# Kernel optimization log

Measured on AMD Instinct MI355X. Metric: run time of the kernel, lower is better.

The kernel has to match this reference:

```python
import jax, jax.numpy as jnp
import numpy as np

# Tap patterns inside the 3x3 window (ky, kx) for each kernel_type.
# kernel_type=0 'skel' (5 taps): cross (center + 4-neighborhood).
SKEL_TAPS = [(0, 1), (1, 0), (1, 1), (1, 2), (2, 1)]


def build_dense_kernel(weight, taps):
    # weight: [O, C, K] sparse-tap weights -> dense [K*O, C, 3, 3] conv kernel,
    # kernel-major channel layout (j*O + o) to match torch.cat over tap dim.
    O, C, K = weight.shape
    dense = jnp.zeros((K, O, C, 3, 3), dtype=weight.dtype)
    for j, (ky, kx) in enumerate(taps):  # K is small and fixed (5)
        dense = dense.at[j, :, :, ky, kx].set(weight[:, :, j])
    return dense.reshape(K * O, C, 3, 3)


def setup_inputs() -> dict:
    key = jax.random.key(0)
    k1, k2 = jax.random.split(key)
    x = jax.random.normal(k1, (32, 128, 64, 64), dtype=jnp.float32)
    weight = jax.random.normal(k2, (128, 128, 5), dtype=jnp.float32) * 0.05
    return {"x": x, "weight": weight}


def reference(x, weight):
    # _SConv forward: sparse-tap conv producing [K, N, O, H, W]; spatial=True
    # concatenates the K per-tap slices along channels -> [N, K*O, H, W].
    # Expressed as a single dense 3x3 conv with zeros at non-tap positions.
    kernel = build_dense_kernel(weight, SKEL_TAPS)  # [K*O, C, 3, 3]
    out = jax.lax.conv_general_dilated(
        x, kernel,
        window_strides=(1, 1),
        padding=((1, 1), (1, 1)),
        rhs_dilation=(1, 1),
        dimension_numbers=("NCHW", "OIHW", "NCHW"),
    )  # [N, K*O, H, W]
    return jax.nn.relu(out)
```

## Files before the change

kernel.cpp:

```cpp
#include <hip/hip_runtime.h>
#include <hip/hip_bf16.h>

typedef __attribute__((ext_vector_type(8))) short bf16x8;
typedef __attribute__((ext_vector_type(4))) float f32x4;

__device__ __forceinline__ short f2bf(float v) {
    unsigned u = __builtin_bit_cast(unsigned, v);
    u += 0x7fffu + ((u >> 16) & 1u);
    return (short)(u >> 16);
}
__device__ __forceinline__ float relu(float v) { return v > 0.f ? v : 0.f; }

__global__ __launch_bounds__(64)
void prep_wfrag(const float* __restrict__ w, bf16x8* __restrict__ wf) {
    const int mt   = blockIdx.x >> 2;
    const int kt   = blockIdx.x & 3;
    const int lane = threadIdx.x;
    const int j  = mt >> 3;
    const int ot = mt & 7;
    const int o  = ot * 16 + (lane & 15);
    const int c0 = kt * 32 + (lane >> 4) * 8;
    const float* wp = w + ((size_t)o * 128 + c0) * 5 + j;
    bf16x8 f;
    #pragma unroll
    for (int e = 0; e < 8; ++e) f[e] = f2bf(wp[e * 5]);
    wf[(size_t)(mt * 4 + kt) * 64 + lane] = f;
}

__global__ __launch_bounds__(512, 4)
void sconv_v4(const float* __restrict__ x, const bf16x8* __restrict__ wf,
              float* __restrict__ out) {
    __shared__ float lds[128 * 64];

    const int bid = blockIdx.x;
    const int h = bid & 63;
    const int n = bid >> 6;

    const int t    = threadIdx.x;
    const int wave = t >> 6;
    const int lane = t & 63;
    const int mh   = wave >> 2;
    const int pt   = wave & 3;
    const int l15  = lane & 15;
    const int lg   = lane >> 4;
    const int pos  = pt * 16 + l15;

    const float* xb = x + (size_t)n * 128 * 4096 + (size_t)(h * 64 + pos);
    bf16x8 xf[4];
    #pragma unroll
    for (int kt = 0; kt < 4; ++kt) {
        const float* xp = xb + (size_t)(kt * 32 + lg * 8) * 4096;
        bf16x8 f;
        #pragma unroll
        for (int e = 0; e < 8; ++e) f[e] = f2bf(xp[(size_t)e * 4096]);
        xf[kt] = f;
    }

    const int wq  = pt * 4 + lg;
    const int wp0 = pt * 16 + lg * 4;

    #pragma unroll
    for (int j = 0; j < 5; ++j) {
        if (j == 1 && t < 128) lds[t * 64 + ((t & 7) << 2)] = 0.f;
        if (j == 3 && t < 128) lds[t * 64 + ((15 ^ (t & 7)) << 2) + 3] = 0.f;

        #pragma unroll
        for (int oi = 0; oi < 4; ++oi) {
            const int ot = mh * 4 + oi;
            const int ch = ot * 16 + l15;
            const bf16x8* wfp = wf + (size_t)((j * 8 + ot) * 4) * 64 + lane;

            f32x4 acc = {0.f, 0.f, 0.f, 0.f};
            #pragma unroll
            for (int kt = 0; kt < 4; ++kt)
                acc = __builtin_amdgcn_mfma_f32_16x16x32_bf16(
                    xf[kt], wfp[(size_t)kt * 64], acc, 0, 0, 0);

            if (j == 0 || j == 2 || j == 4) {
                f32x4 v;
                #pragma unroll
                for (int r = 0; r < 4; ++r) v[r] = relu(acc[r]);
                *reinterpret_cast<f32x4*>(
                    &lds[ch * 64 + ((wq ^ (ch & 7)) << 2)]) = v;
            } else {
                #pragma unroll
                for (int r = 0; r < 4; ++r) {
                    const int ws = wp0 + r + (j == 1 ? 1 : -1);
                    if ((unsigned)ws < 64u)
                        lds[ch * 64 + (((ws >> 2) ^ (ch & 7)) << 2) + (ws & 3)]
                            = relu(acc[r]);
                }
            }
        }
        __syncthreads();

        const int  hs = (j == 0) ? ((h + 1) & 63)
                      : (j == 4) ? ((h + 63) & 63) : h;
        const bool zr = (j == 0 && h == 63) || (j == 4 && h == 0);

        #pragma unroll
        for (int i = 0; i < 4; ++i) {
            const int g  = i * 512 + t;
            const int ch = g >> 4;
            const int q  = g & 15;
            f32x4 v = *reinterpret_cast<const f32x4*>(
                &lds[ch * 64 + ((q ^ (ch & 7)) << 2)]);
            if (zr) v = f32x4{0.f, 0.f, 0.f, 0.f};
            __builtin_nontemporal_store(
                v, reinterpret_cast<f32x4*>(
                       out + (((size_t)n * 640 + j * 128 + ch) * 64 + hs) * 64
                           + q * 4));
        }
        if (j < 4) __syncthreads();
    }
}

__global__ __launch_bounds__(512, 2)
void sconv_mfma(const float* __restrict__ x, const float* __restrict__ w,
                float* __restrict__ out) {
    __shared__ bf16x8 wfrag[8][4][64];
    const int bid = blockIdx.x;
    const int j   = bid % 5;
    const int hp  = (bid / 5) % 32;
    const int n   = bid / 160;
    const int t = threadIdx.x;
    for (int s = t; s < 2048; s += 512) {
        const int lane = s & 63;
        const int rest = s >> 6;
        const int mt   = rest >> 2;
        const int kt   = rest & 3;
        const int o    = mt * 16 + (lane & 15);
        const int c0   = kt * 32 + (lane >> 4) * 8;
        const float* wp = w + ((size_t)o * 128 + c0) * 5 + j;
        bf16x8 f;
        #pragma unroll
        for (int e = 0; e < 8; ++e) f[e] = f2bf(wp[e * 5]);
        wfrag[mt][kt][lane] = f;
    }
    __syncthreads();
    const int wave = t >> 6;
    const int lane = t & 63;
    const int l15  = lane & 15;
    const int lg   = lane >> 4;
    const int h    = hp * 2 + (wave >> 2);
    const int wcol = (wave & 3) * 16 + l15;
    const int dy[5] = {-1, 0, 0, 0, 1};
    const int dx[5] = { 0,-1, 0, 1, 0};
    const int hi = h + dy[j];
    const int wi = wcol + dx[j];
    const bool valid = ((unsigned)hi < 64u) && ((unsigned)wi < 64u);
    const int hic = hi < 0 ? 0 : (hi > 63 ? 63 : hi);
    const int wic = wi < 0 ? 0 : (wi > 63 ? 63 : wi);
    const float* xb = x + (size_t)n * 128 * 4096 + (size_t)(hic * 64 + wic);
    bf16x8 xf[4];
    #pragma unroll
    for (int kt = 0; kt < 4; ++kt) {
        const int c0 = kt * 32 + lg * 8;
        const float* xp = xb + (size_t)c0 * 4096;
        bf16x8 f;
        #pragma unroll
        for (int e = 0; e < 8; ++e) {
            float v = xp[(size_t)e * 4096];
            f[e] = f2bf(valid ? v : 0.0f);
        }
        xf[kt] = f;
    }
    f32x4 acc[8];
    #pragma unroll
    for (int mt = 0; mt < 8; ++mt) acc[mt] = f32x4{0.f, 0.f, 0.f, 0.f};
    #pragma unroll
    for (int kt = 0; kt < 4; ++kt)
        #pragma unroll
        for (int mt = 0; mt < 8; ++mt)
            acc[mt] = __builtin_amdgcn_mfma_f32_16x16x32_bf16(
                wfrag[mt][kt][lane], xf[kt], acc[mt], 0, 0, 0);
    float* ob = out + ((size_t)n * 640 + (size_t)j * 128) * 4096
                    + (size_t)(h * 64 + wcol);
    #pragma unroll
    for (int mt = 0; mt < 8; ++mt) {
        const int ch = mt * 16 + lg * 4;
        #pragma unroll
        for (int r = 0; r < 4; ++r) {
            float v = acc[mt][r];
            ob[(size_t)(ch + r) * 4096] = v > 0.f ? v : 0.f;
        }
    }
}

extern "C" void kernel_launch(void* const* d_in, const int* in_sizes, int n_in,
                              void* d_out, int out_size, void* d_ws, size_t ws_size,
                              hipStream_t stream) {
    const float* x = (const float*)d_in[0];
    const float* w = (const float*)d_in[1];
    float* out = (float*)d_out;

    const size_t wf_bytes = (size_t)40 * 4 * 64 * sizeof(bf16x8);
    if (ws_size >= wf_bytes) {
        bf16x8* wf = (bf16x8*)d_ws;
        hipLaunchKernelGGL(prep_wfrag, dim3(160), dim3(64), 0, stream, w, wf);
        hipLaunchKernelGGL(sconv_v4, dim3(32 * 64), dim3(512), 0, stream,
                           x, wf, out);
    } else {
        hipLaunchKernelGGL(sconv_mfma, dim3(32 * 32 * 5), dim3(512), 0, stream,
                           x, w, out);
    }
}
```

Baseline: 80.10 us.

## Process two output rows per block to reuse weight fragments

Result: no change. 80.31 us (+0.3%).

```diff
diff --git a/kernel.cpp b/kernel.cpp
--- a/kernel.cpp
+++ b/kernel.cpp
@@ -28,13 +28,14 @@
 }
 
 __global__ __launch_bounds__(512, 4)
-void sconv_v4(const float* __restrict__ x, const bf16x8* __restrict__ wf,
+void sconv_v5(const float* __restrict__ x, const bf16x8* __restrict__ wf,
               float* __restrict__ out) {
     __shared__ float lds[128 * 64];
 
     const int bid = blockIdx.x;
-    const int h = bid & 63;
-    const int n = bid >> 6;
+    const int hp = bid & 31;
+    const int n  = bid >> 5;
+    const int h0 = hp * 2;
 
     const int t    = threadIdx.x;
     const int wave = t >> 6;
@@ -45,15 +46,19 @@
     const int lg   = lane >> 4;
     const int pos  = pt * 16 + l15;
 
-    const float* xb = x + (size_t)n * 128 * 4096 + (size_t)(h * 64 + pos);
-    bf16x8 xf[4];
-    #pragma unroll
-    for (int kt = 0; kt < 4; ++kt) {
-        const float* xp = xb + (size_t)(kt * 32 + lg * 8) * 4096;
-        bf16x8 f;
-        #pragma unroll
-        for (int e = 0; e < 8; ++e) f[e] = f2bf(xp[(size_t)e * 4096]);
-        xf[kt] = f;
+    const float* xb = x + (size_t)n * 128 * 4096 + (size_t)(h0 * 64 + pos);
+    bf16x8 xf[2][4];
+    #pragma unroll
+    for (int r = 0; r < 2; ++r) {
+        #pragma unroll
+        for (int kt = 0; kt < 4; ++kt) {
+            const float* xp = xb + (size_t)r * 64
+                            + (size_t)(kt * 32 + lg * 8) * 4096;
+            bf16x8 f;
+            #pragma unroll
+            for (int e = 0; e < 8; ++e) f[e] = f2bf(xp[(size_t)e * 4096]);
+            xf[r][kt] = f;
+        }
     }
 
     const int wq  = pt * 4 + lg;
@@ -61,57 +66,70 @@
 
     #pragma unroll
     for (int j = 0; j < 5; ++j) {
-        if (j == 1 && t < 128) lds[t * 64 + ((t & 7) << 2)] = 0.f;
-        if (j == 3 && t < 128) lds[t * 64 + ((15 ^ (t & 7)) << 2) + 3] = 0.f;
-
+        f32x4 acc[4][2];
         #pragma unroll
         for (int oi = 0; oi < 4; ++oi) {
             const int ot = mh * 4 + oi;
-            const int ch = ot * 16 + l15;
             const bf16x8* wfp = wf + (size_t)((j * 8 + ot) * 4) * 64 + lane;
-
-            f32x4 acc = {0.f, 0.f, 0.f, 0.f};
-            #pragma unroll
-            for (int kt = 0; kt < 4; ++kt)
-                acc = __builtin_amdgcn_mfma_f32_16x16x32_bf16(
-                    xf[kt], wfp[(size_t)kt * 64], acc, 0, 0, 0);
-
-            if (j == 0 || j == 2 || j == 4) {
-                f32x4 v;
-                #pragma unroll
-                for (int r = 0; r < 4; ++r) v[r] = relu(acc[r]);
-                *reinterpret_cast<f32x4*>(
-                    &lds[ch * 64 + ((wq ^ (ch & 7)) << 2)]) = v;
-            } else {
-                #pragma unroll
-                for (int r = 0; r < 4; ++r) {
-                    const int ws = wp0 + r + (j == 1 ? 1 : -1);
-                    if ((unsigned)ws < 64u)
-                        lds[ch * 64 + (((ws >> 2) ^ (ch & 7)) << 2) + (ws & 3)]
-                            = relu(acc[r]);
+            acc[oi][0] = f32x4{0.f, 0.f, 0.f, 0.f};
+            acc[oi][1] = f32x4{0.f, 0.f, 0.f, 0.f};
+            #pragma unroll
+            for (int kt = 0; kt < 4; ++kt) {
+                const bf16x8 b = wfp[(size_t)kt * 64];
+                acc[oi][0] = __builtin_amdgcn_mfma_f32_16x16x32_bf16(
+                    xf[0][kt], b, acc[oi][0], 0, 0, 0);
+                acc[oi][1] = __builtin_amdgcn_mfma_f32_16x16x32_bf16(
+                    xf[1][kt], b, acc[oi][1], 0, 0, 0);
+            }
+        }
+
+        #pragma unroll
+        for (int r = 0; r < 2; ++r) {
+            const int h = h0 + r;
+
+            if (j == 1 && t < 128) lds[t * 64 + ((t & 7) << 2)] = 0.f;
+            if (j == 3 && t < 128) lds[t * 64 + ((15 ^ (t & 7)) << 2) + 3] = 0.f;
+
+            #pragma unroll
+            for (int oi = 0; oi < 4; ++oi) {
+                const int ch = (mh * 4 + oi) * 16 + l15;
+                if (j == 0 || j == 2 || j == 4) {
+                    f32x4 v;
+                    #pragma unroll
+                    for (int q = 0; q < 4; ++q) v[q] = relu(acc[oi][r][q]);
+                    *reinterpret_cast<f32x4*>(
+                        &lds[ch * 64 + ((wq ^ (ch & 7)) << 2)]) = v;
+                } else {
+                    #pragma unroll
+                    for (int q = 0; q < 4; ++q) {
+                        const int ws = wp0 + q + (j == 1 ? 1 : -1);
+                        if ((unsigned)ws < 64u)
+                            lds[ch * 64 + (((ws >> 2) ^ (ch & 7)) << 2) + (ws & 3)]
+                                = relu(acc[oi][r][q]);
+                    }
                 }
             }
-        }
-        __syncthreads();
-
-        const int  hs = (j == 0) ? ((h + 1) & 63)
-                      : (j == 4) ? ((h + 63) & 63) : h;
-        const bool zr = (j == 0 && h == 63) || (j == 4 && h == 0);
-
-        #pragma unroll
-        for (int i = 0; i < 4; ++i) {
-            const int g  = i * 512 + t;
-            const int ch = g >> 4;
-            const int q  = g & 15;
-            f32x4 v = *reinterpret_cast<const f32x4*>(
-                &lds[ch * 64 + ((q ^ (ch & 7)) << 2)]);
-            if (zr) v = f32x4{0.f, 0.f, 0.f, 0.f};
-            __builtin_nontemporal_store(
-                v, reinterpret_cast<f32x4*>(
-                       out + (((size_t)n * 640 + j * 128 + ch) * 64 + hs) * 64
-                           + q * 4));
-        }
-        if (j < 4) __syncthreads();
+            __syncthreads();
+
+            const int  hs = (j == 0) ? ((h + 1) & 63)
+                          : (j == 4) ? ((h + 63) & 63) : h;
+            const bool zr = (j == 0 && h == 63) || (j == 4 && h == 0);
+
+            #pragma unroll
+            for (int i = 0; i < 4; ++i) {
+                const int g  = i * 512 + t;
+                const int ch = g >> 4;
+                const int q  = g & 15;
+                f32x4 v = *reinterpret_cast<const f32x4*>(
+                    &lds[ch * 64 + ((q ^ (ch & 7)) << 2)]);
+                if (zr) v = f32x4{0.f, 0.f, 0.f, 0.f};
+                __builtin_nontemporal_store(
+                    v, reinterpret_cast<f32x4*>(
+                           out + (((size_t)n * 640 + j * 128 + ch) * 64 + hs) * 64
+                               + q * 4));
+            }
+            if (j < 4 || r < 1) __syncthreads();
+        }
     }
 }
 
@@ -198,7 +216,7 @@
     if (ws_size >= wf_bytes) {
         bf16x8* wf = (bf16x8*)d_ws;
         hipLaunchKernelGGL(prep_wfrag, dim3(160), dim3(64), 0, stream, w, wf);
-        hipLaunchKernelGGL(sconv_v4, dim3(32 * 64), dim3(512), 0, stream,
+        hipLaunchKernelGGL(sconv_v5, dim3(32 * 32), dim3(512), 0, stream,
                            x, wf, out);
     } else {
         hipLaunchKernelGGL(sconv_mfma, dim3(32 * 32 * 5), dim3(512), 0, stream,
```

## Process two output rows per block, splitting channels into two halves

Applied to the files above, without the earlier changes.

After: 80.19 us. Within noise of the previous version (+0.1%).

```diff
diff --git a/kernel.cpp b/kernel.cpp
--- a/kernel.cpp
+++ b/kernel.cpp
@@ -10,6 +10,9 @@
     return (short)(u >> 16);
 }
 __device__ __forceinline__ float relu(float v) { return v > 0.f ? v : 0.f; }
+
+#define ROWP 68
+#define CHP  136
 
 __global__ __launch_bounds__(64)
 void prep_wfrag(const float* __restrict__ w, bf16x8* __restrict__ wf) {
@@ -27,23 +30,25 @@
     wf[(size_t)(mt * 4 + kt) * 64 + lane] = f;
 }
 
-__global__ __launch_bounds__(512, 4)
-void sconv_v4(const float* __restrict__ x, const bf16x8* __restrict__ wf,
+__global__ __launch_bounds__(512, 8)
+void sconv_v8(const float* __restrict__ x, const bf16x8* __restrict__ wf,
               float* __restrict__ out) {
-    __shared__ float lds[128 * 64];
+    __shared__ float lds[64 * CHP];
 
     const int bid = blockIdx.x;
-    const int h = bid & 63;
-    const int n = bid >> 6;
+    const int hp = bid & 31;
+    const int n  = bid >> 5;
+    const int h0 = hp * 2;
 
     const int t    = threadIdx.x;
     const int wave = t >> 6;
     const int lane = t & 63;
-    const int mh   = wave >> 2;
-    const int pt   = wave & 3;
     const int l15  = lane & 15;
     const int lg   = lane >> 4;
+    const int r    = wave >> 2;
+    const int pt   = wave & 3;
     const int pos  = pt * 16 + l15;
+    const int h    = h0 + r;
 
     const float* xb = x + (size_t)n * 128 * 4096 + (size_t)(h * 64 + pos);
     bf16x8 xf[4];
@@ -57,61 +62,65 @@
     }
 
     const int wq  = pt * 4 + lg;
-    const int wp0 = pt * 16 + lg * 4;
+    const int wc0 = pt * 16 + lg * 4;
 
     #pragma unroll
     for (int j = 0; j < 5; ++j) {
-        if (j == 1 && t < 128) lds[t * 64 + ((t & 7) << 2)] = 0.f;
-        if (j == 3 && t < 128) lds[t * 64 + ((15 ^ (t & 7)) << 2) + 3] = 0.f;
-
-        #pragma unroll
-        for (int oi = 0; oi < 4; ++oi) {
-            const int ot = mh * 4 + oi;
-            const int ch = ot * 16 + l15;
-            const bf16x8* wfp = wf + (size_t)((j * 8 + ot) * 4) * 64 + lane;
-
-            f32x4 acc = {0.f, 0.f, 0.f, 0.f};
+        #pragma unroll
+        for (int p = 0; p < 2; ++p) {
+            if (j == 1 && t < 128)
+                lds[(t >> 1) * CHP + (t & 1) * ROWP + 0] = 0.f;
+            if (j == 3 && t < 128)
+                lds[(t >> 1) * CHP + (t & 1) * ROWP + 63] = 0.f;
+
             #pragma unroll
-            for (int kt = 0; kt < 4; ++kt)
-                acc = __builtin_amdgcn_mfma_f32_16x16x32_bf16(
-                    xf[kt], wfp[(size_t)kt * 64], acc, 0, 0, 0);
-
-            if (j == 0 || j == 2 || j == 4) {
-                f32x4 v;
+            for (int oi = 0; oi < 4; ++oi) {
+                const int ot = p * 4 + oi;
+                const int cl = oi * 16 + l15;
+                const bf16x8* wfp = wf + (size_t)((j * 8 + ot) * 4) * 64 + lane;
+                f32x4 acc = {0.f, 0.f, 0.f, 0.f};
                 #pragma unroll
-                for (int r = 0; r < 4; ++r) v[r] = relu(acc[r]);
-                *reinterpret_cast<f32x4*>(
-                    &lds[ch * 64 + ((wq ^ (ch & 7)) << 2)]) = v;
-            } else {
-                #pragma unroll
-                for (int r = 0; r < 4; ++r) {
-                    const int ws = wp0 + r + (j == 1 ? 1 : -1);
-                    if ((unsigned)ws < 64u)
-                        lds[ch * 64 + (((ws >> 2) ^ (ch & 7)) << 2) + (ws & 3)]
-                            = relu(acc[r]);
+                for (int kt = 0; kt < 4; ++kt)
+                    acc = __builtin_amdgcn_mfma_f32_16x16x32_bf16(
+                        xf[kt], wfp[(size_t)kt * 64], acc, 0, 0, 0);
+
+                if (j == 0 || j == 2 || j == 4) {
+                    f32x4 v;
+                    #pragma unroll
+                    for (int q = 0; q < 4; ++q) v[q] = relu(acc[q]);
+                    *reinterpret_cast<f32x4*>(
+                        &lds[cl * CHP + r * ROWP + wq * 4]) = v;
+                } else {
+                    #pragma unroll
+                    for (int q = 0; q < 4; ++q) {
+                        const int ws = wc0 + q + (j == 1 ? 1 : -1);
+                        if ((unsigned)ws < 64u)
+                            lds[cl * CHP + r * ROWP + ws] = relu(acc[q]);
+                    }
                 }
             }
+            __syncthreads();
+
+            #pragma unroll
+            for (int i = 0; i < 4; ++i) {
+                const int g  = i * 512 + t;
+                const int cl = g >> 5;
+                const int hr = (g >> 4) & 1;
+                const int q  = g & 15;
+                f32x4 v = *reinterpret_cast<const f32x4*>(
+                    &lds[cl * CHP + hr * ROWP + q * 4]);
+                const int hh = h0 + hr;
+                const int hs = (j == 0) ? ((hh + 1) & 63)
+                             : (j == 4) ? ((hh + 63) & 63) : hh;
+                if ((j == 0 && hh == 63) || (j == 4 && hh == 0))
+                    v = f32x4{0.f, 0.f, 0.f, 0.f};
+                __builtin_nontemporal_store(
+                    v, reinterpret_cast<f32x4*>(
+                           out + (((size_t)n * 640 + j * 128 + p * 64 + cl) * 64
+                                  + hs) * 64 + q * 4));
+            }
+            if (j < 4 || p < 1) __syncthreads();
         }
-        __syncthreads();
-
-        const int  hs = (j == 0) ? ((h + 1) & 63)
-                      : (j == 4) ? ((h + 63) & 63) : h;
-        const bool zr = (j == 0 && h == 63) || (j == 4 && h == 0);
-
-        #pragma unroll
-        for (int i = 0; i < 4; ++i) {
-            const int g  = i * 512 + t;
-            const int ch = g >> 4;
-            const int q  = g & 15;
-            f32x4 v = *reinterpret_cast<const f32x4*>(
-                &lds[ch * 64 + ((q ^ (ch & 7)) << 2)]);
-            if (zr) v = f32x4{0.f, 0.f, 0.f, 0.f};
-            __builtin_nontemporal_store(
-                v, reinterpret_cast<f32x4*>(
-                       out + (((size_t)n * 640 + j * 128 + ch) * 64 + hs) * 64
-                           + q * 4));
-        }
-        if (j < 4) __syncthreads();
     }
 }
 
@@ -198,7 +207,7 @@
     if (ws_size >= wf_bytes) {
         bf16x8* wf = (bf16x8*)d_ws;
         hipLaunchKernelGGL(prep_wfrag, dim3(160), dim3(64), 0, stream, w, wf);
-        hipLaunchKernelGGL(sconv_v4, dim3(32 * 64), dim3(512), 0, stream,
+        hipLaunchKernelGGL(sconv_v8, dim3(32 * 32), dim3(512), 0, stream,
                            x, wf, out);
     } else {
         hipLaunchKernelGGL(sconv_mfma, dim3(32 * 32 * 5), dim3(512), 0, stream,
```
